# Kernel optimization log

Measured on AMD Instinct MI355X. Metric: run time of the kernel, lower is better.

The kernel has to match this reference:

```python
import jax, jax.numpy as jnp
import numpy as np

N = 50000      # nodes
D = 128        # in = hidden = out channels
L = 3          # num_layers
E = 320000     # edges per edge type
EPS_BN = 1e-5
EPS_NORM = 1e-12


def setup_inputs() -> dict:
    key = jax.random.key(0)
    ks = jax.random.split(key, 16)
    s = 1.0 / np.sqrt(D)
    inp = {}
    inp['x'] = jax.random.normal(ks[0], (N, D), jnp.float32)
    inp['edge_index0'] = jax.random.randint(ks[1], (2, E), 0, N, jnp.int32)
    inp['edge_index1'] = jax.random.randint(ks[2], (2, E), 0, N, jnp.int32)
    inp['W0'] = jax.random.normal(ks[3], (L, D, D), jnp.float32) * s
    inp['b0'] = jnp.zeros((L, D), jnp.float32)
    inp['W1'] = jax.random.normal(ks[4], (L, D, D), jnp.float32) * s
    inp['b1'] = jnp.zeros((L, D), jnp.float32)
    inp['gamma'] = jnp.ones((L, D), jnp.float32)
    inp['beta'] = jnp.zeros((L, D), jnp.float32)
    inp['emb1_W'] = jax.random.normal(ks[5], (D, D), jnp.float32) * s
    inp['emb1_b'] = jnp.zeros((D,), jnp.float32)
    inp['emb2_W'] = jax.random.normal(ks[6], (D, D), jnp.float32) * s
    inp['emb2_b'] = jnp.zeros((D,), jnp.float32)
    inp['ph1_Wa'] = jax.random.normal(ks[7], (D, D), jnp.float32) * s
    inp['ph1_ba'] = jnp.zeros((D,), jnp.float32)
    inp['ph1_Wb'] = jax.random.normal(ks[8], (D, D), jnp.float32) * s
    inp['ph1_bb'] = jnp.zeros((D,), jnp.float32)
    inp['ph2_Wa'] = jax.random.normal(ks[9], (D, D), jnp.float32) * s
    inp['ph2_ba'] = jnp.zeros((D,), jnp.float32)
    inp['ph2_Wb'] = jax.random.normal(ks[10], (D, D), jnp.float32) * s
    inp['ph2_bb'] = jnp.zeros((D,), jnp.float32)
    return inp


def _gcn(h_in, W, b, src, dst):
    # PyG GCNConv: add self-loops, symmetric deg^{-1/2} normalization, then scatter-add.
    h = h_in @ W                                   # [N, D]
    ones = jnp.ones(src.shape[0], h.dtype)
    deg = jax.ops.segment_sum(ones, dst, num_segments=N) + 1.0   # +1 self-loop
    dinv = jax.lax.rsqrt(deg)
    coef = (dinv[src] * dinv[dst])[:, None]        # [E, 1]
    agg = jax.ops.segment_sum(h[src] * coef, dst, num_segments=N)
    agg = agg + h * (dinv * dinv)[:, None]         # self-loop contribution
    return agg + b


def _bn(x, g, bt):
    # training-mode BatchNorm1d (batch statistics, biased variance)
    mu = jnp.mean(x, axis=0)
    var = jnp.mean(jnp.square(x - mu), axis=0)
    return (x - mu) * jax.lax.rsqrt(var + EPS_BN) * g + bt


def _l2norm(x):
    n = jnp.sqrt(jnp.sum(x * x, axis=1, keepdims=True))
    return x / jnp.maximum(n, EPS_NORM)


def reference(x, edge_index0, edge_index1, W0, b0, W1, b1, gamma, beta,
              emb1_W, emb1_b, emb2_W, emb2_b,
              ph1_Wa, ph1_ba, ph1_Wb, ph1_bb,
              ph2_Wa, ph2_ba, ph2_Wb, ph2_bb):
    s0, d0 = edge_index0[0], edge_index0[1]
    s1, d1 = edge_index1[0], edge_index1[1]
    h = x
    for i in range(L):
        # HeteroConv with aggr='sum': sum of the two edge-type GCNConv outputs
        h = _gcn(h, W0[i], b0[i], s0, d0) + _gcn(h, W1[i], b1[i], s1, d1)
        h = _bn(h, gamma[i], beta[i])
        if i < L - 1:
            h = jax.nn.relu(h)   # dropout omitted (deterministic / eval)
    e1 = jnp.tanh(h @ emb1_W + emb1_b)
    e2 = _l2norm(jnp.tanh(h @ emb2_W + emb2_b))
    p1 = _l2norm(jax.nn.relu(e1 @ ph1_Wa + ph1_ba) @ ph1_Wb + ph1_bb)
    p2 = _l2norm(jax.nn.relu(e2 @ ph2_Wa + ph2_ba) @ ph2_Wb + ph2_bb)
    return (e1, e2, p1, p2)
```

## Files before the change

### kernel.cpp

```cpp
#include <hip/hip_runtime.h>
#include <cstdint>
#include <cstddef>

#define D 128

typedef __attribute__((ext_vector_type(8))) short bf16x8;
typedef __attribute__((ext_vector_type(4))) float f32x4;
typedef __attribute__((ext_vector_type(8))) _Float16 f16x8;

__device__ __forceinline__ unsigned short f2bf(float f) {
  unsigned int u = __float_as_uint(f);
  unsigned int r = u + 0x7FFFu + ((u >> 16) & 1u);
  return (unsigned short)(r >> 16);
}
__device__ __forceinline__ float bf2f(unsigned short h) {
  return __uint_as_float((unsigned int)h << 16);
}
__device__ __forceinline__ float fast_tanh(float x) {
  float cx = fminf(fmaxf(x, -15.f), 15.f);
  float e = __expf(2.f * cx);
  return (e - 1.f) * __builtin_amdgcn_rcpf(e + 1.f);
}
union HU { _Float16 f; unsigned short u; };

struct WPtrs { const float* w[12]; };

__global__ __launch_bounds__(256) void packcount_kernel(
    WPtrs P, unsigned short* __restrict__ Wp,
    const int* __restrict__ d0, const int* __restrict__ d1,
    int* __restrict__ cnt, int E, int N, int packBlocks) {
  if ((int)blockIdx.x < packBlocks) {
    int tid = blockIdx.x * 256 + threadIdx.x;
    int m = tid >> 14;
    int r = tid & 16383;
    int b = r & 7, lane = (r >> 3) & 63, ks = (r >> 9) & 3, jt = r >> 11;
    int k = ks * 32 + ((lane >> 4) << 3) + b;
    int j = jt * 16 + (lane & 15);
    float w = P.w[m][k * 128 + j];
    if (m < 8) {
      unsigned short h = f2bf(w);
      Wp[m * 32768 + r] = h;
      Wp[m * 32768 + 16384 + r] = f2bf(w - bf2f(h));
    } else {
      HU hh, ll;
      hh.f = (_Float16)w;
      ll.f = (_Float16)(w - (float)hh.f);
      Wp[m * 32768 + r] = hh.u;
      Wp[m * 32768 + 16384 + r] = ll.u;
    }
  } else {
    int e = ((int)blockIdx.x - packBlocks) * 256 + threadIdx.x;
    if (e < E) {
      atomicAdd(&cnt[d0[e]], 1);
      atomicAdd(&cnt[N + d1[e]], 1);
    }
  }
}

__global__ __launch_bounds__(256) void scan_part_kernel(const int* __restrict__ cnt,
                                                        int* __restrict__ off,
                                                        int* __restrict__ bsum, int n2) {
  __shared__ int sh[256];
  int t = threadIdx.x;
  int i0 = blockIdx.x * 512 + 2 * t;
  int a0 = (i0 < n2) ? cnt[i0] : 0;
  int a1 = (i0 + 1 < n2) ? cnt[i0 + 1] : 0;
  int s = a0 + a1;
  sh[t] = s;
  __syncthreads();
  for (int d = 1; d < 256; d <<= 1) {
    int v = (t >= d) ? sh[t - d] : 0;
    __syncthreads();
    sh[t] += v;
    __syncthreads();
  }
  int p = sh[t] - s;
  if (i0 < n2) off[i0] = p;
  if (i0 + 1 < n2) off[i0 + 1] = p + a0;
  if (t == 255) bsum[blockIdx.x] = sh[255];
}

__global__ __launch_bounds__(256) void scan_bsum_kernel(int* __restrict__ bsum, int nb,
                                                        int* __restrict__ off_total) {
  __shared__ int sh[256];
  int t = threadIdx.x;
  int s = (t < nb) ? bsum[t] : 0;
  sh[t] = s;
  __syncthreads();
  for (int d = 1; d < 256; d <<= 1) {
    int v = (t >= d) ? sh[t - d] : 0;
    __syncthreads();
    sh[t] += v;
    __syncthreads();
  }
  if (t < nb) bsum[t] = sh[t] - s;
  if (t == 255) *off_total = sh[255];
}

__global__ __launch_bounds__(256) void scan_add_kernel(int* __restrict__ off,
                                                       const int* __restrict__ bsum,
                                                       int* __restrict__ cnt,
                                                       float* __restrict__ dinv, int n2) {
  int add = bsum[blockIdx.x];
  int base = blockIdx.x * 512;
#pragma unroll
  for (int u = 0; u < 2; u++) {
    int i = base + threadIdx.x + u * 256;
    if (i < n2) {
      off[i] += add;
      dinv[i] = rsqrtf((float)cnt[i] + 1.0f);
      cnt[i] = 0;
    }
  }
}

__device__ __forceinline__ void split8(const float vv[8], bf16x8& hh, bf16x8& hl) {
#pragma unroll
  for (int c = 0; c < 8; c++) {
    unsigned short h = f2bf(vv[c]);
    hh[c] = (short)h;
    hl[c] = (short)f2bf(vv[c] - bf2f(h));
  }
}

template <int BN>
__device__ __forceinline__ void mm_dual_body(
    int bid, const unsigned short* __restrict__ Wp, const float* __restrict__ Af,
    const float* __restrict__ stats, const float* __restrict__ g0,
    const float* __restrict__ bt0, const float* __restrict__ dinv,
    _Float16* __restrict__ tab0, _Float16* __restrict__ tab1,
    int n, int N, float invn) {
  __shared__ float bnsc[128], bnsh[128];
  if (BN) {
    int t = threadIdx.x;
    if (t < 128) {
      float s = 0.f, q = 0.f;
#pragma unroll
      for (int r = 0; r < 8; r++) { s += stats[r * 128 + t]; q += stats[1024 + r * 128 + t]; }
      float mu = s * invn, var = q * invn - mu * mu;
      float sc = g0[t] * rsqrtf(var + 1e-5f);
      bnsc[t] = sc; bnsh[t] = bt0[t] - mu * sc;
    }
    __syncthreads();
  }
  constexpr int WJT = 4, WIT = 4;
  const int lane = threadIdx.x & 63;
  const int wid = threadIdx.x >> 6;
  const int wj = wid % 4, wi = wid / 4;
  const int jtbase = wj * WJT;
  const int ibase = bid * 64 + wi * WIT * 16;
  const int lrow = lane & 15, lgrp = lane >> 4;

  int node[WIT];
  bool valid[WIT];
#pragma unroll
  for (int it = 0; it < WIT; it++) {
    int i = ibase + it * 16 + lrow;
    valid[it] = (i < n);
    node[it] = valid[it] ? i : (n - 1);
  }

  f32x4 acc[WJT][WIT];
#pragma unroll
  for (int jt = 0; jt < WJT; jt++)
#pragma unroll
    for (int it = 0; it < WIT; it++) acc[jt][it] = (f32x4){0.f, 0.f, 0.f, 0.f};

#pragma unroll
  for (int ks = 0; ks < 4; ks++) {
    float sck[8], shk[8];
    if (BN) {
      int cb = ks * 32 + lgrp * 8;
#pragma unroll
      for (int c = 0; c < 8; c++) { sck[c] = bnsc[cb + c]; shk[c] = bnsh[cb + c]; }
    }
    bf16x8 awh[WJT], awl[WJT];
#pragma unroll
    for (int jt = 0; jt < WJT; jt++) {
      int jg = jtbase + jt;
      const unsigned short* base = Wp + ((jg >= 8) ? 32768 : 0);
      size_t fo = (size_t)(((jg & 7) * 4 + ks) * 64 + lane) * 8;
      awh[jt] = *(const bf16x8*)(base + fo);
      awl[jt] = *(const bf16x8*)(base + fo + 16384);
    }
#pragma unroll
    for (int it = 0; it < WIT; it++) {
      const float* src = Af + (size_t)node[it] * 128 + ks * 32 + lgrp * 8;
      float4 u0 = *(const float4*)src;
      float4 u1 = *(const float4*)(src + 4);
      float vv[8] = {u0.x, u0.y, u0.z, u0.w, u1.x, u1.y, u1.z, u1.w};
      if (BN) {
#pragma unroll
        for (int c = 0; c < 8; c++) vv[c] = fmaxf(vv[c] * sck[c] + shk[c], 0.f);
      }
      bf16x8 bhh, bhl;
      split8(vv, bhh, bhl);
#pragma unroll
      for (int jt = 0; jt < WJT; jt++) {
        acc[jt][it] = __builtin_amdgcn_mfma_f32_16x16x32_bf16(awh[jt], bhh, acc[jt][it], 0, 0, 0);
        acc[jt][it] = __builtin_amdgcn_mfma_f32_16x16x32_bf16(awl[jt], bhh, acc[jt][it], 0, 0, 0);
        acc[jt][it] = __builtin_amdgcn_mfma_f32_16x16x32_bf16(awh[jt], bhl, acc[jt][it], 0, 0, 0);
      }
    }
  }

#pragma unroll
  for (int it = 0; it < WIT; it++) {
    if (!valid[it]) continue;
    float d0v = dinv[node[it]];
    float d1v = dinv[N + node[it]];
#pragma unroll
    for (int jt = 0; jt < WJT; jt++) {
      int jg = jtbase + jt;
      float s = (jg < 8) ? d0v : d1v;
      _Float16 o[4];
#pragma unroll
      for (int c = 0; c < 4; c++) o[c] = (_Float16)(acc[jt][it][c] * s);
      _Float16* base = (jg < 8)
          ? (tab0 + (size_t)node[it] * 128 + jg * 16)
          : (tab1 + (size_t)node[it] * 128 + (jg - 8) * 16);
      *(uint2*)(base + lgrp * 4) = *(uint2*)o;
    }
  }
}

__global__ __launch_bounds__(256) void mm_dual_k(
    const unsigned short* __restrict__ Wp, const float* __restrict__ Af,
    const float* __restrict__ stats, const float* __restrict__ g0,
    const float* __restrict__ bt0, const float* __restrict__ dinv,
    _Float16* __restrict__ tab0, _Float16* __restrict__ tab1,
    int n, int N, float invn) {
  mm_dual_body<1>(blockIdx.x, Wp, Af, stats, g0, bt0, dinv, tab0, tab1, n, N, invn);
}

__global__ __launch_bounds__(256) void fillmm0_kernel(
    const int* __restrict__ ei0, const int* __restrict__ ei1,
    const int* __restrict__ off, int* __restrict__ cnt, int* __restrict__ csr,
    int E, int fillBlocks,
    const unsigned short* __restrict__ Wp, const float* __restrict__ x,
    const float* __restrict__ dinv, _Float16* __restrict__ tab0,
    _Float16* __restrict__ tab1, int n, int N) {
  if ((int)blockIdx.x < fillBlocks) {
    int e = blockIdx.x * 256 + threadIdx.x;
    if (e < E) {
      int s = ei0[e], d = ei0[E + e];
      int p = atomicAdd(&cnt[d], 1);
      csr[off[d] + p] = s;
      s = ei1[e]; d = ei1[E + e];
      p = atomicAdd(&cnt[N + d], 1);
      csr[off[N + d] + p] = s;
    }
  } else {
    mm_dual_body<0>(blockIdx.x - fillBlocks, Wp, x, nullptr, nullptr, nullptr,
                    dinv, tab0, tab1, n, N, 0.f);
  }
}

__global__ __launch_bounds__(256) void gather_kernel(
    const _Float16* __restrict__ tab0, const _Float16* __restrict__ tab1,
    const float* __restrict__ dinv, const int* __restrict__ off,
    const int* __restrict__ csr,
    const float* __restrict__ b0, const float* __restrict__ b1,
    float* __restrict__ outh, float* __restrict__ stats, int n, int N) {
  __shared__ float reds[4][128];
  __shared__ float redq[4][128];
  int t = threadIdx.x;
  int g = t >> 4, l = t & 15;
  int node = blockIdx.x * 16 + g;
  bool valid = node < n;
  int nd = valid ? node : 0;
  const f16x8* t0 = (const f16x8*)tab0;
  const f16x8* t1 = (const f16x8*)tab1;
  float s0[8] = {0,0,0,0,0,0,0,0}, s1[8] = {0,0,0,0,0,0,0,0};
  if (valid) {
    f16x8 v = t0[(size_t)nd * 16 + l];
#pragma unroll
    for (int c = 0; c < 8; c++) s0[c] = (float)v[c];
    v = t1[(size_t)nd * 16 + l];
#pragma unroll
    for (int c = 0; c < 8; c++) s1[c] = (float)v[c];
  }
  int a = valid ? off[nd] : 0, b = valid ? off[nd + 1] : 0;
  int j = a;
  for (; j + 3 < b; j += 4) {
    int i0 = csr[j], i1 = csr[j + 1], i2 = csr[j + 2], i3 = csr[j + 3];
    f16x8 v0 = t0[(size_t)i0 * 16 + l];
    f16x8 v1 = t0[(size_t)i1 * 16 + l];
    f16x8 v2 = t0[(size_t)i2 * 16 + l];
    f16x8 v3 = t0[(size_t)i3 * 16 + l];
#pragma unroll
    for (int c = 0; c < 8; c++)
      s0[c] += ((float)v0[c] + (float)v1[c]) + ((float)v2[c] + (float)v3[c]);
  }
  for (; j < b; j++) {
    f16x8 va = t0[(size_t)csr[j] * 16 + l];
#pragma unroll
    for (int c = 0; c < 8; c++) s0[c] += (float)va[c];
  }
  a = valid ? off[N + nd] : 0; b = valid ? off[N + nd + 1] : 0;
  j = a;
  for (; j + 3 < b; j += 4) {
    int i0 = csr[j], i1 = csr[j + 1], i2 = csr[j + 2], i3 = csr[j + 3];
    f16x8 v0 = t1[(size_t)i0 * 16 + l];
    f16x8 v1 = t1[(size_t)i1 * 16 + l];
    f16x8 v2 = t1[(size_t)i2 * 16 + l];
    f16x8 v3 = t1[(size_t)i3 * 16 + l];
#pragma unroll
    for (int c = 0; c < 8; c++)
      s1[c] += ((float)v0[c] + (float)v1[c]) + ((float)v2[c] + (float)v3[c]);
  }
  for (; j < b; j++) {
    f16x8 va = t1[(size_t)csr[j] * 16 + l];
#pragma unroll
    for (int c = 0; c < 8; c++) s1[c] += (float)va[c];
  }
  float o[8] = {0,0,0,0,0,0,0,0};
  if (valid) {
    float d0 = dinv[nd], d1 = dinv[N + nd];
    const float4* B0 = (const float4*)(b0 + l * 8);
    const float4* B1 = (const float4*)(b1 + l * 8);
    float4 ba0 = B0[0], ba1 = B0[1], bb0 = B1[0], bb1 = B1[1];
    float bs[8] = {ba0.x + bb0.x, ba0.y + bb0.y, ba0.z + bb0.z, ba0.w + bb0.w,
                   ba1.x + bb1.x, ba1.y + bb1.y, ba1.z + bb1.z, ba1.w + bb1.w};
#pragma unroll
    for (int c = 0; c < 8; c++) o[c] = d0 * s0[c] + d1 * s1[c] + bs[c];
    float* dst = outh + (size_t)nd * 128 + l * 8;
    *(float4*)dst = make_float4(o[0], o[1], o[2], o[3]);
    *(float4*)(dst + 4) = make_float4(o[4], o[5], o[6], o[7]);
  }
  float sv[8], q[8];
#pragma unroll
  for (int c = 0; c < 8; c++) { sv[c] = o[c]; q[c] = o[c] * o[c]; }
#pragma unroll
  for (int c = 0; c < 8; c++) {
    sv[c] += __shfl_xor(sv[c], 16); sv[c] += __shfl_xor(sv[c], 32);
    q[c] += __shfl_xor(q[c], 16);  q[c] += __shfl_xor(q[c], 32);
  }
  int lane = t & 63, wid = t >> 6;
  if (lane < 16) {
#pragma unroll
    for (int c = 0; c < 8; c++) { reds[wid][lane * 8 + c] = sv[c]; redq[wid][lane * 8 + c] = q[c]; }
  }
  __syncthreads();
  if (t < 128) {
    float ts = reds[0][t] + reds[1][t] + reds[2][t] + reds[3][t];
    float tq = redq[0][t] + redq[1][t] + redq[2][t] + redq[3][t];
    int cp = blockIdx.x & 7;
    atomicAdd(&stats[cp * 128 + t], ts);
    atomicAdd(&stats[1024 + cp * 128 + t], tq);
  }
}

#define TPH 136
__global__ __launch_bounds__(256) void heads3_kernel(
    const unsigned short* __restrict__ Wp,
    const float* __restrict__ h, const float* __restrict__ stats,
    const float* __restrict__ g2, const float* __restrict__ bt2,
    const float* __restrict__ emb1_b, const float* __restrict__ emb2_b,
    const float* __restrict__ ph1_ba, const float* __restrict__ ph1_bb,
    const float* __restrict__ ph2_ba, const float* __restrict__ ph2_bb,
    float* __restrict__ out, int n, float invn) {
  __shared__ float bnsc[128], bnsh[128];
  __shared__ _Float16 tile[2][64 * TPH];
  __shared__ float l2red[2][4][16][2];
  const int t = threadIdx.x;
  if (t < 128) {
    float s = 0.f, q = 0.f;
#pragma unroll
    for (int r = 0; r < 8; r++) { s += stats[r * 128 + t]; q += stats[1024 + r * 128 + t]; }
    float mu = s * invn, var = q * invn - mu * mu;
    float sc = g2[t] * rsqrtf(var + 1e-5f);
    bnsc[t] = sc; bnsh[t] = bt2[t] - mu * sc;
  }
  __syncthreads();

  const int lane = t & 63, wid = t >> 6;
  const int wj = wid & 1, wh = wid >> 1;
  const int lrow = lane & 15, lgrp = lane >> 4;
  const int jtbase = wj * 4;
  const int base = blockIdx.x * 64;
  const size_t ND = (size_t)n * 128;
  _Float16* myt = &tile[wh][0];

  int node[4];
  bool valid[4];
#pragma unroll
  for (int it = 0; it < 4; it++) {
    int i = base + it * 16 + lrow;
    valid[it] = (i < n);
    node[it] = valid[it] ? i : (n - 1);
  }

  f32x4 acc[4][4];
  const unsigned short* slot;
  const float* bias;

  slot = Wp + (size_t)(6 + wh) * 32768;
  bias = wh ? emb2_b : emb1_b;
#pragma unroll
  for (int jt = 0; jt < 4; jt++) {
    float4 b4 = *(const float4*)(bias + (jtbase + jt) * 16 + lgrp * 4);
#pragma unroll
    for (int it = 0; it < 4; it++) acc[jt][it] = (f32x4){b4.x, b4.y, b4.z, b4.w};
  }
#pragma unroll
  for (int ks = 0; ks < 4; ks++) {
    int cb = ks * 32 + lgrp * 8;
    float sck[8], shk[8];
#pragma unroll
    for (int c = 0; c < 8; c++) { sck[c] = bnsc[cb + c]; shk[c] = bnsh[cb + c]; }
    bf16x8 awh[4], awl[4];
#pragma unroll
    for (int jt = 0; jt < 4; jt++) {
      size_t fo = (size_t)(((jtbase + jt) * 4 + ks) * 64 + lane) * 8;
      awh[jt] = *(const bf16x8*)(slot + fo);
      awl[jt] = *(const bf16x8*)(slot + fo + 16384);
    }
#pragma unroll
    for (int it = 0; it < 4; it++) {
      const float* src = h + (size_t)node[it] * 128 + cb;
      float4 u0 = *(const float4*)src;
      float4 u1 = *(const float4*)(src + 4);
      float vv[8] = {u0.x, u0.y, u0.z, u0.w, u1.x, u1.y, u1.z, u1.w};
#pragma unroll
      for (int c = 0; c < 8; c++) vv[c] = vv[c] * sck[c] + shk[c];
      bf16x8 bhh, bhl;
      split8(vv, bhh, bhl);
#pragma unroll
      for (int jt = 0; jt < 4; jt++) {
        acc[jt][it] = __builtin_amdgcn_mfma_f32_16x16x32_bf16(awh[jt], bhh, acc[jt][it], 0, 0, 0);
        acc[jt][it] = __builtin_amdgcn_mfma_f32_16x16x32_bf16(awl[jt], bhh, acc[jt][it], 0, 0, 0);
        acc[jt][it] = __builtin_amdgcn_mfma_f32_16x16x32_bf16(awh[jt], bhl, acc[jt][it], 0, 0, 0);
      }
    }
  }
#pragma unroll
  for (int jt = 0; jt < 4; jt++)
#pragma unroll
    for (int it = 0; it < 4; it++)
#pragma unroll
      for (int c = 0; c < 4; c++) acc[jt][it][c] = fast_tanh(acc[jt][it][c]);

  float rsv[4];
  if (wh == 1) {
#pragma unroll
    for (int it = 0; it < 4; it++) {
      float rs = 0.f;
#pragma unroll
      for (int jt = 0; jt < 4; jt++)
#pragma unroll
        for (int c = 0; c < 4; c++) rs += acc[jt][it][c] * acc[jt][it][c];
      rs += __shfl_xor(rs, 16);
      rs += __shfl_xor(rs, 32);
      rsv[it] = rs;
      if (lane < 16) l2red[1][it][lane][wj] = rs;
    }
  }
  __syncthreads();
  if (wh == 1) {
#pragma unroll
    for (int it = 0; it < 4; it++) {
      float full = rsv[it] + l2red[1][it][lrow][wj ^ 1];
      float scl = 1.f / fmaxf(sqrtf(full), 1e-12f);
#pragma unroll
      for (int jt = 0; jt < 4; jt++)
#pragma unroll
        for (int c = 0; c < 4; c++) acc[jt][it][c] *= scl;
    }
  }
#pragma unroll
  for (int it = 0; it < 4; it++) {
#pragma unroll
    for (int jt = 0; jt < 4; jt++) {
      if (valid[it])
        *(float4*)(out + (size_t)wh * ND + (size_t)node[it] * 128 + (jtbase + jt) * 16 + lgrp * 4) =
            make_float4(acc[jt][it][0], acc[jt][it][1], acc[jt][it][2], acc[jt][it][3]);
      _Float16 o4[4];
#pragma unroll
      for (int c = 0; c < 4; c++) o4[c] = (_Float16)acc[jt][it][c];
      *(uint2*)(myt + (it * 16 + lrow) * TPH + (jtbase + jt) * 16 + lgrp * 4) = *(uint2*)o4;
    }
  }
  __syncthreads();

  slot = Wp + (size_t)(8 + 2 * wh) * 32768;
  bias = wh ? ph2_ba : ph1_ba;
#pragma unroll
  for (int jt = 0; jt < 4; jt++) {
    float4 b4 = *(const float4*)(bias + (jtbase + jt) * 16 + lgrp * 4);
#pragma unroll
    for (int it = 0; it < 4; it++) acc[jt][it] = (f32x4){b4.x, b4.y, b4.z, b4.w};
  }
#pragma unroll
  for (int ks = 0; ks < 4; ks++) {
    f16x8 awh[4], awl[4];
#pragma unroll
    for (int jt = 0; jt < 4; jt++) {
      size_t fo = (size_t)(((jtbase + jt) * 4 + ks) * 64 + lane) * 8;
      awh[jt] = *(const f16x8*)(slot + fo);
      awl[jt] = *(const f16x8*)(slot + fo + 16384);
    }
#pragma unroll
    for (int it = 0; it < 4; it++) {
      f16x8 bh = *(const f16x8*)(myt + (it * 16 + lrow) * TPH + ks * 32 + lgrp * 8);
#pragma unroll
      for (int jt = 0; jt < 4; jt++) {
        acc[jt][it] = __builtin_amdgcn_mfma_f32_16x16x32_f16(awh[jt], bh, acc[jt][it], 0, 0, 0);
        acc[jt][it] = __builtin_amdgcn_mfma_f32_16x16x32_f16(awl[jt], bh, acc[jt][it], 0, 0, 0);
      }
    }
  }
#pragma unroll
  for (int jt = 0; jt < 4; jt++)
#pragma unroll
    for (int it = 0; it < 4; it++)
#pragma unroll
      for (int c = 0; c < 4; c++) acc[jt][it][c] = fmaxf(acc[jt][it][c], 0.f);
  __syncthreads();
#pragma unroll
  for (int it = 0; it < 4; it++)
#pragma unroll
    for (int jt = 0; jt < 4; jt++) {
      _Float16 o4[4];
#pragma unroll
      for (int c = 0; c < 4; c++) o4[c] = (_Float16)acc[jt][it][c];
      *(uint2*)(myt + (it * 16 + lrow) * TPH + (jtbase + jt) * 16 + lgrp * 4) = *(uint2*)o4;
    }
  __syncthreads();

  slot = Wp + (size_t)(9 + 2 * wh) * 32768;
  bias = wh ? ph2_bb : ph1_bb;
#pragma unroll
  for (int jt = 0; jt < 4; jt++) {
    float4 b4 = *(const float4*)(bias + (jtbase + jt) * 16 + lgrp * 4);
#pragma unroll
    for (int it = 0; it < 4; it++) acc[jt][it] = (f32x4){b4.x, b4.y, b4.z, b4.w};
  }
#pragma unroll
  for (int ks = 0; ks < 4; ks++) {
    f16x8 awh[4], awl[4];
#pragma unroll
    for (int jt = 0; jt < 4; jt++) {
      size_t fo = (size_t)(((jtbase + jt) * 4 + ks) * 64 + lane) * 8;
      awh[jt] = *(const f16x8*)(slot + fo);
      awl[jt] = *(const f16x8*)(slot + fo + 16384);
    }
#pragma unroll
    for (int it = 0; it < 4; it++) {
      f16x8 bh = *(const f16x8*)(myt + (it * 16 + lrow) * TPH + ks * 32 + lgrp * 8);
#pragma unroll
      for (int jt = 0; jt < 4; jt++) {
        acc[jt][it] = __builtin_amdgcn_mfma_f32_16x16x32_f16(awh[jt], bh, acc[jt][it], 0, 0, 0);
        acc[jt][it] = __builtin_amdgcn_mfma_f32_16x16x32_f16(awl[jt], bh, acc[jt][it], 0, 0, 0);
      }
    }
  }
#pragma unroll
  for (int it = 0; it < 4; it++) {
    float rs = 0.f;
#pragma unroll
    for (int jt = 0; jt < 4; jt++)
#pragma unroll
      for (int c = 0; c < 4; c++) rs += acc[jt][it][c] * acc[jt][it][c];
    rs += __shfl_xor(rs, 16);
    rs += __shfl_xor(rs, 32);
    rsv[it] = rs;
    if (lane < 16) l2red[wh][it][lane][wj] = rs;
  }
  __syncthreads();
#pragma unroll
  for (int it = 0; it < 4; it++) {
    float full = rsv[it] + l2red[wh][it][lrow][wj ^ 1];
    float scl = 1.f / fmaxf(sqrtf(full), 1e-12f);
    if (!valid[it]) continue;
#pragma unroll
    for (int jt = 0; jt < 4; jt++)
      *(float4*)(out + (size_t)(2 + wh) * ND + (size_t)node[it] * 128 + (jtbase + jt) * 16 + lgrp * 4) =
          make_float4(acc[jt][it][0] * scl, acc[jt][it][1] * scl,
                      acc[jt][it][2] * scl, acc[jt][it][3] * scl);
  }
}

extern "C" void kernel_launch(void* const* d_in, const int* in_sizes, int n_in,
                              void* d_out, int out_size, void* d_ws, size_t ws_size,
                              hipStream_t stream) {
  const float* x      = (const float*)d_in[0];
  const int*   ei0    = (const int*)d_in[1];
  const int*   ei1    = (const int*)d_in[2];
  const float* W0     = (const float*)d_in[3];
  const float* b0     = (const float*)d_in[4];
  const float* W1     = (const float*)d_in[5];
  const float* b1     = (const float*)d_in[6];
  const float* gamma  = (const float*)d_in[7];
  const float* beta   = (const float*)d_in[8];
  const float* emb1_W = (const float*)d_in[9];
  const float* emb1_b = (const float*)d_in[10];
  const float* emb2_W = (const float*)d_in[11];
  const float* emb2_b = (const float*)d_in[12];
  const float* ph1_Wa = (const float*)d_in[13];
  const float* ph1_ba = (const float*)d_in[14];
  const float* ph1_Wb = (const float*)d_in[15];
  const float* ph1_bb = (const float*)d_in[16];
  const float* ph2_Wa = (const float*)d_in[17];
  const float* ph2_ba = (const float*)d_in[18];
  const float* ph2_Wb = (const float*)d_in[19];
  const float* ph2_bb = (const float*)d_in[20];

  const int N = in_sizes[0] / D;
  const int E = in_sizes[1] / 2;
  const int N2 = 2 * N;
  const size_t ND = (size_t)N * D;
  const float invn = 1.0f / (float)N;
  float* out = (float*)d_out;

  char* p = (char*)d_ws;
  auto carve = [&](size_t bytes) -> void* {
    void* r = (void*)p;
    p += (bytes + 255) & ~(size_t)255;
    return r;
  };
  int*   cnt   = (int*)carve((size_t)N2 * 4);
  float* stats = (float*)carve((size_t)3 * 2048 * 4);
  size_t zbytes = (size_t)((char*)(stats + 3 * 2048) - (char*)cnt);
  int*   off   = (int*)carve((size_t)(N2 + 1) * 4);
  float* dinv  = (float*)carve((size_t)N2 * 4);
  int*   csr   = (int*)carve((size_t)2 * E * 4);
  int*   bsum  = (int*)carve(256 * 4);
  unsigned short* Wp = (unsigned short*)carve((size_t)12 * 32768 * 2);
  float* hbuf = (float*)carve(4 * ND);
  _Float16* tab0 = (_Float16*)carve(2 * ND);
  _Float16* tab1 = (_Float16*)carve(2 * ND);

  const int TPB = 256;
  const int packBlocks = 768;
  const int gridPC = packBlocks + (E + TPB - 1) / TPB;
  const int fillBlocks = (E + TPB - 1) / TPB;
  const int nbScan = (N2 + 511) / 512;
  const int gridDual = (N + 63) / 64;
  const int gridGath = (N + 15) / 16;
  const int gridH3 = (N + 63) / 64;

  WPtrs P;
  P.w[0] = W0;                     P.w[1] = W1;
  P.w[2] = W0 + (size_t)D * D;     P.w[3] = W1 + (size_t)D * D;
  P.w[4] = W0 + (size_t)2 * D * D; P.w[5] = W1 + (size_t)2 * D * D;
  P.w[6] = emb1_W; P.w[7] = emb2_W;
  P.w[8] = ph1_Wa; P.w[9] = ph1_Wb;
  P.w[10] = ph2_Wa; P.w[11] = ph2_Wb;

  hipMemsetAsync(cnt, 0, zbytes, stream);
  packcount_kernel<<<gridPC, TPB, 0, stream>>>(P, Wp, ei0 + E, ei1 + E, cnt, E, N, packBlocks);
  scan_part_kernel<<<nbScan, TPB, 0, stream>>>(cnt, off, bsum, N2);
  scan_bsum_kernel<<<1, TPB, 0, stream>>>(bsum, nbScan, off + N2);
  scan_add_kernel<<<nbScan, TPB, 0, stream>>>(off, bsum, cnt, dinv, N2);

  fillmm0_kernel<<<fillBlocks + gridDual, TPB, 0, stream>>>(
      ei0, ei1, off, cnt, csr, E, fillBlocks, Wp, x, dinv, tab0, tab1, N, N);
  gather_kernel<<<gridGath, TPB, 0, stream>>>(tab0, tab1, dinv, off, csr,
                                              b0, b1, hbuf, stats, N, N);
  for (int i = 1; i < 3; i++) {
    mm_dual_k<<<gridDual, TPB, 0, stream>>>(Wp + (size_t)(2 * i) * 32768, hbuf,
                                            stats + (size_t)(i - 1) * 2048,
                                            gamma + (i - 1) * D, beta + (i - 1) * D,
                                            dinv, tab0, tab1, N, N, invn);
    gather_kernel<<<gridGath, TPB, 0, stream>>>(tab0, tab1, dinv, off, csr,
                                                b0 + i * D, b1 + i * D, hbuf,
                                                stats + (size_t)i * 2048, N, N);
  }

  heads3_kernel<<<gridH3, TPB, 0, stream>>>(
      Wp, hbuf, stats + (size_t)2 * 2048, gamma + 2 * D, beta + 2 * D,
      emb1_b, emb2_b, ph1_ba, ph1_bb, ph2_ba, ph2_bb, out, N, invn);
}
```

Before: 329.1 us.

## Sort nodes by total degree so gather blocks process similar-degree nodes

Adds a degree histogram, a scan over its bins and an atomic bucket scatter that builds a node permutation ordered by combined in-degree. The gather kernel then handles nodes in that order, so the 16-node groups within a block have similar loop trip counts and less load imbalance. The cost is two extra kernel launches, atomics, an indirection read per node, and output writes plus neighbour-table reads that are less coalesced because consecutive groups now touch scattered node ids.

New measurement: 484.5 us. 47.2% more time.

```diff
diff --git a/kernel.cpp b/kernel.cpp
--- a/kernel.cpp
+++ b/kernel.cpp
@@ -114,6 +114,53 @@
   }
 }
 
+__global__ __launch_bounds__(256) void fillhist_kernel(
+    const int* __restrict__ ei0, const int* __restrict__ ei1,
+    const int* __restrict__ off, int* __restrict__ cnt,
+    int* __restrict__ csr, int* __restrict__ hist,
+    int E, int N, int fillBlocks, int histBlocks) {
+  if ((int)blockIdx.x < fillBlocks) {
+    int e = blockIdx.x * 256 + threadIdx.x;
+    if (e < E) {
+      int s = ei0[e], d = ei0[E + e];
+      int p = atomicAdd(&cnt[d], 1);
+      csr[off[d] + p] = s;
+      s = ei1[e]; d = ei1[E + e];
+      p = atomicAdd(&cnt[N + d], 1);
+      csr[off[N + d] + p] = s;
+    }
+  } else {
+    __shared__ int lh[512];
+    int t = threadIdx.x;
+    lh[t] = 0; lh[t + 256] = 0;
+    __syncthreads();
+    int stride = histBlocks * 256;
+    for (int i = ((int)blockIdx.x - fillBlocks) * 256 + t; i < N; i += stride) {
+      int key = (off[i + 1] - off[i]) + (off[N + i + 1] - off[N + i]);
+      atomicAdd(&lh[key < 511 ? key : 511], 1);
+    }
+    __syncthreads();
+    if (lh[t]) atomicAdd(&hist[t], lh[t]);
+    if (lh[t + 256]) atomicAdd(&hist[t + 256], lh[t + 256]);
+  }
+}
+
+__global__ __launch_bounds__(512) void binscan_kernel(const int* __restrict__ hist,
+                                                      int* __restrict__ cursor) {
+  __shared__ int sh[512];
+  int t = threadIdx.x;
+  int s = hist[t];
+  sh[t] = s;
+  __syncthreads();
+  for (int d = 1; d < 512; d <<= 1) {
+    int v = (t >= d) ? sh[t - d] : 0;
+    __syncthreads();
+    sh[t] += v;
+    __syncthreads();
+  }
+  cursor[t] = sh[t] - s;
+}
+
 __device__ __forceinline__ void split8(const float vv[8], bf16x8& hh, bf16x8& hl) {
 #pragma unroll
   for (int c = 0; c < 8; c++) {
@@ -233,25 +280,22 @@
   mm_dual_body<1>(blockIdx.x, Wp, Af, stats, g0, bt0, dinv, tab0, tab1, n, N, invn);
 }
 
-__global__ __launch_bounds__(256) void fillmm0_kernel(
-    const int* __restrict__ ei0, const int* __restrict__ ei1,
-    const int* __restrict__ off, int* __restrict__ cnt, int* __restrict__ csr,
-    int E, int fillBlocks,
+__global__ __launch_bounds__(256) void scatmm0_kernel(
+    const int* __restrict__ off, int* __restrict__ cursor, int* __restrict__ order,
+    int sortBlocks,
     const unsigned short* __restrict__ Wp, const float* __restrict__ x,
     const float* __restrict__ dinv, _Float16* __restrict__ tab0,
     _Float16* __restrict__ tab1, int n, int N) {
-  if ((int)blockIdx.x < fillBlocks) {
-    int e = blockIdx.x * 256 + threadIdx.x;
-    if (e < E) {
-      int s = ei0[e], d = ei0[E + e];
-      int p = atomicAdd(&cnt[d], 1);
-      csr[off[d] + p] = s;
-      s = ei1[e]; d = ei1[E + e];
-      p = atomicAdd(&cnt[N + d], 1);
-      csr[off[N + d] + p] = s;
+  if ((int)blockIdx.x < sortBlocks) {
+    int stride = sortBlocks * 256;
+    for (int i = (int)blockIdx.x * 256 + threadIdx.x; i < N; i += stride) {
+      int key = (off[i + 1] - off[i]) + (off[N + i + 1] - off[N + i]);
+      int b = key < 511 ? key : 511;
+      int pos = atomicAdd(&cursor[b], 1);
+      order[pos] = i;
     }
   } else {
-    mm_dual_body<0>(blockIdx.x - fillBlocks, Wp, x, nullptr, nullptr, nullptr,
+    mm_dual_body<0>(blockIdx.x - sortBlocks, Wp, x, nullptr, nullptr, nullptr,
                     dinv, tab0, tab1, n, N, 0.f);
   }
 }
@@ -259,16 +303,16 @@
 __global__ __launch_bounds__(256) void gather_kernel(
     const _Float16* __restrict__ tab0, const _Float16* __restrict__ tab1,
     const float* __restrict__ dinv, const int* __restrict__ off,
-    const int* __restrict__ csr,
+    const int* __restrict__ csr, const int* __restrict__ order,
     const float* __restrict__ b0, const float* __restrict__ b1,
     float* __restrict__ outh, float* __restrict__ stats, int n, int N) {
   __shared__ float reds[4][128];
   __shared__ float redq[4][128];
   int t = threadIdx.x;
   int g = t >> 4, l = t & 15;
-  int node = blockIdx.x * 16 + g;
-  bool valid = node < n;
-  int nd = valid ? node : 0;
+  int pos = blockIdx.x * 16 + g;
+  bool valid = pos < n;
+  int nd = valid ? order[pos] : 0;
   const f16x8* t0 = (const f16x8*)tab0;
   const f16x8* t1 = (const f16x8*)tab1;
   float s0[8] = {0,0,0,0,0,0,0,0}, s1[8] = {0,0,0,0,0,0,0,0};
@@ -621,7 +665,10 @@
   };
   int*   cnt   = (int*)carve((size_t)N2 * 4);
   float* stats = (float*)carve((size_t)3 * 2048 * 4);
-  size_t zbytes = (size_t)((char*)(stats + 3 * 2048) - (char*)cnt);
+  int*   hist  = (int*)carve(512 * 4);
+  size_t zbytes = (size_t)((char*)(hist + 512) - (char*)cnt);
+  int*   cursor = (int*)carve(512 * 4);
+  int*   order  = (int*)carve((size_t)N * 4);
   int*   off   = (int*)carve((size_t)(N2 + 1) * 4);
   float* dinv  = (float*)carve((size_t)N2 * 4);
   int*   csr   = (int*)carve((size_t)2 * E * 4);
@@ -635,6 +682,8 @@
   const int packBlocks = 768;
   const int gridPC = packBlocks + (E + TPB - 1) / TPB;
   const int fillBlocks = (E + TPB - 1) / TPB;
+  const int histBlocks = 32;
+  const int sortBlocks = 32;
   const int nbScan = (N2 + 511) / 512;
   const int gridDual = (N + 63) / 64;
   const int gridGath = (N + 15) / 16;
@@ -653,21 +702,22 @@
   scan_part_kernel<<<nbScan, TPB, 0, stream>>>(cnt, off, bsum, N2);
   scan_bsum_kernel<<<1, TPB, 0, stream>>>(bsum, nbScan, off + N2);
   scan_add_kernel<<<nbScan, TPB, 0, stream>>>(off, bsum, cnt, dinv, N2);
-
-  fillmm0_kernel<<<fillBlocks + gridDual, TPB, 0, stream>>>(
-      ei0, ei1, off, cnt, csr, E, fillBlocks, Wp, x, dinv, tab0, tab1, N, N);
-  gather_kernel<<<gridGath, TPB, 0, stream>>>(tab0, tab1, dinv, off, csr,
+  fillhist_kernel<<<fillBlocks + histBlocks, TPB, 0, stream>>>(
+      ei0, ei1, off, cnt, csr, hist, E, N, fillBlocks, histBlocks);
+  binscan_kernel<<<1, 512, 0, stream>>>(hist, cursor);
+  scatmm0_kernel<<<sortBlocks + gridDual, TPB, 0, stream>>>(
+      off, cursor, order, sortBlocks, Wp, x, dinv, tab0, tab1, N, N);
+  gather_kernel<<<gridGath, TPB, 0, stream>>>(tab0, tab1, dinv, off, csr, order,
                                               b0, b1, hbuf, stats, N, N);
   for (int i = 1; i < 3; i++) {
     mm_dual_k<<<gridDual, TPB, 0, stream>>>(Wp + (size_t)(2 * i) * 32768, hbuf,
                                             stats + (size_t)(i - 1) * 2048,
                                             gamma + (i - 1) * D, beta + (i - 1) * D,
                                             dinv, tab0, tab1, N, N, invn);
-    gather_kernel<<<gridGath, TPB, 0, stream>>>(tab0, tab1, dinv, off, csr,
+    gather_kernel<<<gridGath, TPB, 0, stream>>>(tab0, tab1, dinv, off, csr, order,
                                                 b0 + i * D, b1 + i * D, hbuf,
                                                 stats + (size_t)i * 2048, N, N);
   }
-
   heads3_kernel<<<gridH3, TPB, 0, stream>>>(
       Wp, hbuf, stats + (size_t)2 * 2048, gamma + 2 * D, beta + 2 * D,
       emb1_b, emb2_b, ph1_ba, ph1_bb, ph2_ba, ph2_bb, out, N, invn);
```

## Split fused fill/matmul kernel and interleave both edge-type gathers in one loop

Applied to the files above, without the earlier changes.

The combined CSR-fill plus first-layer matmul launch is split back into a separate fill kernel and a templated mm_dual kernel launched on its own. The gather kernel now walks both edge types' neighbor lists in one predicated loop, issuing four loads from each table per iteration to raise memory-level parallelism. Splitting the launches adds one kernel launch and removes overlap between the fill and matmul blocks. The interleaved loop wastes loads on padded lanes when one list is shorter than the other.

New measurement: 348.5 us. +5.9%, slower.

```diff
diff --git a/kernel.cpp b/kernel.cpp
--- a/kernel.cpp
+++ b/kernel.cpp
@@ -114,6 +114,20 @@
   }
 }
 
+__global__ void fill_kernel(const int* __restrict__ ei0, const int* __restrict__ ei1,
+                            const int* __restrict__ off, int* __restrict__ cnt,
+                            int* __restrict__ csr, int E, int N) {
+  int e = blockIdx.x * blockDim.x + threadIdx.x;
+  if (e < E) {
+    int s = ei0[e], d = ei0[E + e];
+    int p = atomicAdd(&cnt[d], 1);
+    csr[off[d] + p] = s;
+    s = ei1[e]; d = ei1[E + e];
+    p = atomicAdd(&cnt[N + d], 1);
+    csr[off[N + d] + p] = s;
+  }
+}
+
 __device__ __forceinline__ void split8(const float vv[8], bf16x8& hh, bf16x8& hl) {
 #pragma unroll
   for (int c = 0; c < 8; c++) {
@@ -124,8 +138,8 @@
 }
 
 template <int BN>
-__device__ __forceinline__ void mm_dual_body(
-    int bid, const unsigned short* __restrict__ Wp, const float* __restrict__ Af,
+__global__ __launch_bounds__(256) void mm_dual(
+    const unsigned short* __restrict__ Wp, const float* __restrict__ Af,
     const float* __restrict__ stats, const float* __restrict__ g0,
     const float* __restrict__ bt0, const float* __restrict__ dinv,
     _Float16* __restrict__ tab0, _Float16* __restrict__ tab1,
@@ -148,7 +162,7 @@
   const int wid = threadIdx.x >> 6;
   const int wj = wid % 4, wi = wid / 4;
   const int jtbase = wj * WJT;
-  const int ibase = bid * 64 + wi * WIT * 16;
+  const int ibase = blockIdx.x * 64 + wi * WIT * 16;
   const int lrow = lane & 15, lgrp = lane >> 4;
 
   int node[WIT];
@@ -221,38 +235,6 @@
           : (tab1 + (size_t)node[it] * 128 + (jg - 8) * 16);
       *(uint2*)(base + lgrp * 4) = *(uint2*)o;
     }
-  }
-}
-
-__global__ __launch_bounds__(256) void mm_dual_k(
-    const unsigned short* __restrict__ Wp, const float* __restrict__ Af,
-    const float* __restrict__ stats, const float* __restrict__ g0,
-    const float* __restrict__ bt0, const float* __restrict__ dinv,
-    _Float16* __restrict__ tab0, _Float16* __restrict__ tab1,
-    int n, int N, float invn) {
-  mm_dual_body<1>(blockIdx.x, Wp, Af, stats, g0, bt0, dinv, tab0, tab1, n, N, invn);
-}
-
-__global__ __launch_bounds__(256) void fillmm0_kernel(
-    const int* __restrict__ ei0, const int* __restrict__ ei1,
-    const int* __restrict__ off, int* __restrict__ cnt, int* __restrict__ csr,
-    int E, int fillBlocks,
-    const unsigned short* __restrict__ Wp, const float* __restrict__ x,
-    const float* __restrict__ dinv, _Float16* __restrict__ tab0,
-    _Float16* __restrict__ tab1, int n, int N) {
-  if ((int)blockIdx.x < fillBlocks) {
-    int e = blockIdx.x * 256 + threadIdx.x;
-    if (e < E) {
-      int s = ei0[e], d = ei0[E + e];
-      int p = atomicAdd(&cnt[d], 1);
-      csr[off[d] + p] = s;
-      s = ei1[e]; d = ei1[E + e];
-      p = atomicAdd(&cnt[N + d], 1);
-      csr[off[N + d] + p] = s;
-    }
-  } else {
-    mm_dual_body<0>(blockIdx.x - fillBlocks, Wp, x, nullptr, nullptr, nullptr,
-                    dinv, tab0, tab1, n, N, 0.f);
   }
 }
 
@@ -280,39 +262,38 @@
 #pragma unroll
     for (int c = 0; c < 8; c++) s1[c] = (float)v[c];
   }
-  int a = valid ? off[nd] : 0, b = valid ? off[nd + 1] : 0;
-  int j = a;
-  for (; j + 3 < b; j += 4) {
-    int i0 = csr[j], i1 = csr[j + 1], i2 = csr[j + 2], i3 = csr[j + 3];
-    f16x8 v0 = t0[(size_t)i0 * 16 + l];
-    f16x8 v1 = t0[(size_t)i1 * 16 + l];
-    f16x8 v2 = t0[(size_t)i2 * 16 + l];
-    f16x8 v3 = t0[(size_t)i3 * 16 + l];
-#pragma unroll
-    for (int c = 0; c < 8; c++)
-      s0[c] += ((float)v0[c] + (float)v1[c]) + ((float)v2[c] + (float)v3[c]);
-  }
-  for (; j < b; j++) {
-    f16x8 va = t0[(size_t)csr[j] * 16 + l];
-#pragma unroll
-    for (int c = 0; c < 8; c++) s0[c] += (float)va[c];
-  }
-  a = valid ? off[N + nd] : 0; b = valid ? off[N + nd + 1] : 0;
-  j = a;
-  for (; j + 3 < b; j += 4) {
-    int i0 = csr[j], i1 = csr[j + 1], i2 = csr[j + 2], i3 = csr[j + 3];
-    f16x8 v0 = t1[(size_t)i0 * 16 + l];
-    f16x8 v1 = t1[(size_t)i1 * 16 + l];
-    f16x8 v2 = t1[(size_t)i2 * 16 + l];
-    f16x8 v3 = t1[(size_t)i3 * 16 + l];
-#pragma unroll
-    for (int c = 0; c < 8; c++)
-      s1[c] += ((float)v0[c] + (float)v1[c]) + ((float)v2[c] + (float)v3[c]);
-  }
-  for (; j < b; j++) {
-    f16x8 va = t1[(size_t)csr[j] * 16 + l];
-#pragma unroll
-    for (int c = 0; c < 8; c++) s1[c] += (float)va[c];
+  int j0 = valid ? off[nd] : 0, e0 = valid ? off[nd + 1] : 0;
+  int j1 = valid ? off[N + nd] : 0, e1 = valid ? off[N + nd + 1] : 0;
+  while (j0 < e0 || j1 < e1) {
+    int idx0[4], idx1[4];
+    bool p0[4], p1[4];
+#pragma unroll
+    for (int k = 0; k < 4; k++) {
+      int jj = j0 + k;
+      p0[k] = jj < e0;
+      idx0[k] = nd;
+      if (p0[k]) idx0[k] = csr[jj];
+      jj = j1 + k;
+      p1[k] = jj < e1;
+      idx1[k] = nd;
+      if (p1[k]) idx1[k] = csr[jj];
+    }
+    f16x8 v0[4], v1[4];
+#pragma unroll
+    for (int k = 0; k < 4; k++) {
+      v0[k] = t0[(size_t)idx0[k] * 16 + l];
+      v1[k] = t1[(size_t)idx1[k] * 16 + l];
+    }
+#pragma unroll
+    for (int k = 0; k < 4; k++) {
+#pragma unroll
+      for (int c = 0; c < 8; c++) {
+        s0[c] += p0[k] ? (float)v0[k][c] : 0.f;
+        s1[c] += p1[k] ? (float)v1[k][c] : 0.f;
+      }
+    }
+    j0 = (j0 + 4 < e0) ? j0 + 4 : e0;
+    j1 = (j1 + 4 < e1) ? j1 + 4 : e1;
   }
   float o[8] = {0,0,0,0,0,0,0,0};
   if (valid) {
@@ -634,7 +615,7 @@
   const int TPB = 256;
   const int packBlocks = 768;
   const int gridPC = packBlocks + (E + TPB - 1) / TPB;
-  const int fillBlocks = (E + TPB - 1) / TPB;
+  const int gridE = (E + TPB - 1) / TPB;
   const int nbScan = (N2 + 511) / 512;
   const int gridDual = (N + 63) / 64;
   const int gridGath = (N + 15) / 16;
@@ -653,21 +634,21 @@
   scan_part_kernel<<<nbScan, TPB, 0, stream>>>(cnt, off, bsum, N2);
   scan_bsum_kernel<<<1, TPB, 0, stream>>>(bsum, nbScan, off + N2);
   scan_add_kernel<<<nbScan, TPB, 0, stream>>>(off, bsum, cnt, dinv, N2);
-
-  fillmm0_kernel<<<fillBlocks + gridDual, TPB, 0, stream>>>(
-      ei0, ei1, off, cnt, csr, E, fillBlocks, Wp, x, dinv, tab0, tab1, N, N);
+  fill_kernel<<<gridE, TPB, 0, stream>>>(ei0, ei1, off, cnt, csr, E, N);
+
+  mm_dual<0><<<gridDual, TPB, 0, stream>>>(Wp, x, nullptr, nullptr, nullptr,
+                                           dinv, tab0, tab1, N, N, invn);
   gather_kernel<<<gridGath, TPB, 0, stream>>>(tab0, tab1, dinv, off, csr,
                                               b0, b1, hbuf, stats, N, N);
   for (int i = 1; i < 3; i++) {
-    mm_dual_k<<<gridDual, TPB, 0, stream>>>(Wp + (size_t)(2 * i) * 32768, hbuf,
-                                            stats + (size_t)(i - 1) * 2048,
-                                            gamma + (i - 1) * D, beta + (i - 1) * D,
-                                            dinv, tab0, tab1, N, N, invn);
+    mm_dual<1><<<gridDual, TPB, 0, stream>>>(Wp + (size_t)(2 * i) * 32768, hbuf,
+                                             stats + (size_t)(i - 1) * 2048,
+                                             gamma + (i - 1) * D, beta + (i - 1) * D,
+                                             dinv, tab0, tab1, N, N, invn);
     gather_kernel<<<gridGath, TPB, 0, stream>>>(tab0, tab1, dinv, off, csr,
                                                 b0 + i * D, b1 + i * D, hbuf,
                                                 stats + (size_t)i * 2048, N, N);
   }
-
   heads3_kernel<<<gridH3, TPB, 0, stream>>>(
       Wp, hbuf, stats + (size_t)2 * 2048, gamma + 2 * D, beta + 2 * D,
       emb1_b, emb2_b, ph1_ba, ph1_bb, ph2_ba, ph2_bb, out, N, invn);
```

## Record atomic ranks in count pass, merge scan kernels, use packed bf16 convert

Applied to the files above, without the earlier changes.

The counting pass now stores the slot returned by each atomicAdd as a per-edge rank, so the CSR fill no longer repeats atomics and instead writes directly at off[d]+rank. The block-sum scan and the add pass are merged into one kernel that every block recomputes redundantly, which removes one launch and the cnt reset. The bf16 hi/lo split is rewritten with the packed v_cvt_pk_bf16_f32 instruction in place of manual rounding. The cost is two extra E-sized int arrays that are written and then read back.

Result: faster. 310.9 us (-5.5%).

```diff
diff --git a/kernel.cpp b/kernel.cpp
--- a/kernel.cpp
+++ b/kernel.cpp
@@ -7,6 +7,7 @@
 typedef __attribute__((ext_vector_type(8))) short bf16x8;
 typedef __attribute__((ext_vector_type(4))) float f32x4;
 typedef __attribute__((ext_vector_type(8))) _Float16 f16x8;
+typedef __attribute__((ext_vector_type(4))) unsigned int u32x4;
 
 __device__ __forceinline__ unsigned short f2bf(float f) {
   unsigned int u = __float_as_uint(f);
@@ -23,12 +24,30 @@
 }
 union HU { _Float16 f; unsigned short u; };
 
+__device__ __forceinline__ void split8(const float vv[8], bf16x8& hh, bf16x8& hl) {
+  u32x4 ph, pl;
+#pragma unroll
+  for (int i = 0; i < 4; i++) {
+    unsigned int p;
+    asm("v_cvt_pk_bf16_f32 %0, %1, %2" : "=v"(p) : "v"(vv[2 * i]), "v"(vv[2 * i + 1]));
+    ph[i] = p;
+    float r0 = vv[2 * i] - __uint_as_float(p << 16);
+    float r1 = vv[2 * i + 1] - __uint_as_float(p & 0xFFFF0000u);
+    unsigned int q;
+    asm("v_cvt_pk_bf16_f32 %0, %1, %2" : "=v"(q) : "v"(r0), "v"(r1));
+    pl[i] = q;
+  }
+  hh = __builtin_bit_cast(bf16x8, ph);
+  hl = __builtin_bit_cast(bf16x8, pl);
+}
+
 struct WPtrs { const float* w[12]; };
 
 __global__ __launch_bounds__(256) void packcount_kernel(
     WPtrs P, unsigned short* __restrict__ Wp,
     const int* __restrict__ d0, const int* __restrict__ d1,
-    int* __restrict__ cnt, int E, int N, int packBlocks) {
+    int* __restrict__ cnt, int* __restrict__ rank0, int* __restrict__ rank1,
+    int E, int N, int packBlocks) {
   if ((int)blockIdx.x < packBlocks) {
     int tid = blockIdx.x * 256 + threadIdx.x;
     int m = tid >> 14;
@@ -51,8 +70,8 @@
   } else {
     int e = ((int)blockIdx.x - packBlocks) * 256 + threadIdx.x;
     if (e < E) {
-      atomicAdd(&cnt[d0[e]], 1);
-      atomicAdd(&cnt[N + d1[e]], 1);
+      rank0[e] = atomicAdd(&cnt[d0[e]], 1);
+      rank1[e] = atomicAdd(&cnt[N + d1[e]], 1);
     }
   }
 }
@@ -80,8 +99,11 @@
   if (t == 255) bsum[blockIdx.x] = sh[255];
 }
 
-__global__ __launch_bounds__(256) void scan_bsum_kernel(int* __restrict__ bsum, int nb,
-                                                        int* __restrict__ off_total) {
+__global__ __launch_bounds__(256) void scan_addm_kernel(int* __restrict__ off,
+                                                        const int* __restrict__ bsum,
+                                                        const int* __restrict__ cnt,
+                                                        float* __restrict__ dinv,
+                                                        int n2, int nb) {
   __shared__ int sh[256];
   int t = threadIdx.x;
   int s = (t < nb) ? bsum[t] : 0;
@@ -93,33 +115,16 @@
     sh[t] += v;
     __syncthreads();
   }
-  if (t < nb) bsum[t] = sh[t] - s;
-  if (t == 255) *off_total = sh[255];
-}
-
-__global__ __launch_bounds__(256) void scan_add_kernel(int* __restrict__ off,
-                                                       const int* __restrict__ bsum,
-                                                       int* __restrict__ cnt,
-                                                       float* __restrict__ dinv, int n2) {
-  int add = bsum[blockIdx.x];
+  if (blockIdx.x == 0 && t == 0) off[n2] = sh[nb - 1];
+  int add = (blockIdx.x > 0) ? sh[blockIdx.x - 1] : 0;
   int base = blockIdx.x * 512;
 #pragma unroll
   for (int u = 0; u < 2; u++) {
-    int i = base + threadIdx.x + u * 256;
+    int i = base + t + u * 256;
     if (i < n2) {
       off[i] += add;
       dinv[i] = rsqrtf((float)cnt[i] + 1.0f);
-      cnt[i] = 0;
-    }
-  }
-}
-
-__device__ __forceinline__ void split8(const float vv[8], bf16x8& hh, bf16x8& hl) {
-#pragma unroll
-  for (int c = 0; c < 8; c++) {
-    unsigned short h = f2bf(vv[c]);
-    hh[c] = (short)h;
-    hl[c] = (short)f2bf(vv[c] - bf2f(h));
+    }
   }
 }
 
@@ -235,7 +240,8 @@
 
 __global__ __launch_bounds__(256) void fillmm0_kernel(
     const int* __restrict__ ei0, const int* __restrict__ ei1,
-    const int* __restrict__ off, int* __restrict__ cnt, int* __restrict__ csr,
+    const int* __restrict__ off, const int* __restrict__ rank0,
+    const int* __restrict__ rank1, int* __restrict__ csr,
     int E, int fillBlocks,
     const unsigned short* __restrict__ Wp, const float* __restrict__ x,
     const float* __restrict__ dinv, _Float16* __restrict__ tab0,
@@ -244,11 +250,9 @@
     int e = blockIdx.x * 256 + threadIdx.x;
     if (e < E) {
       int s = ei0[e], d = ei0[E + e];
-      int p = atomicAdd(&cnt[d], 1);
-      csr[off[d] + p] = s;
+      csr[off[d] + rank0[e]] = s;
       s = ei1[e]; d = ei1[E + e];
-      p = atomicAdd(&cnt[N + d], 1);
-      csr[off[N + d] + p] = s;
+      csr[off[N + d] + rank1[e]] = s;
     }
   } else {
     mm_dual_body<0>(blockIdx.x - fillBlocks, Wp, x, nullptr, nullptr, nullptr,
@@ -625,6 +629,8 @@
   int*   off   = (int*)carve((size_t)(N2 + 1) * 4);
   float* dinv  = (float*)carve((size_t)N2 * 4);
   int*   csr   = (int*)carve((size_t)2 * E * 4);
+  int*   rank0 = (int*)carve((size_t)E * 4);
+  int*   rank1 = (int*)carve((size_t)E * 4);
   int*   bsum  = (int*)carve(256 * 4);
   unsigned short* Wp = (unsigned short*)carve((size_t)12 * 32768 * 2);
   float* hbuf = (float*)carve(4 * ND);
@@ -649,13 +655,13 @@
   P.w[10] = ph2_Wa; P.w[11] = ph2_Wb;
 
   hipMemsetAsync(cnt, 0, zbytes, stream);
-  packcount_kernel<<<gridPC, TPB, 0, stream>>>(P, Wp, ei0 + E, ei1 + E, cnt, E, N, packBlocks);
+  packcount_kernel<<<gridPC, TPB, 0, stream>>>(P, Wp, ei0 + E, ei1 + E, cnt,
+                                               rank0, rank1, E, N, packBlocks);
   scan_part_kernel<<<nbScan, TPB, 0, stream>>>(cnt, off, bsum, N2);
-  scan_bsum_kernel<<<1, TPB, 0, stream>>>(bsum, nbScan, off + N2);
-  scan_add_kernel<<<nbScan, TPB, 0, stream>>>(off, bsum, cnt, dinv, N2);
+  scan_addm_kernel<<<nbScan, TPB, 0, stream>>>(off, bsum, cnt, dinv, N2, nbScan);
 
   fillmm0_kernel<<<fillBlocks + gridDual, TPB, 0, stream>>>(
-      ei0, ei1, off, cnt, csr, E, fillBlocks, Wp, x, dinv, tab0, tab1, N, N);
+      ei0, ei1, off, rank0, rank1, csr, E, fillBlocks, Wp, x, dinv, tab0, tab1, N, N);
   gather_kernel<<<gridGath, TPB, 0, stream>>>(tab0, tab1, dinv, off, csr,
                                               b0, b1, hbuf, stats, N, N);
   for (int i = 1; i < 3; i++) {
@@ -667,7 +673,6 @@
                                                 b0 + i * D, b1 + i * D, hbuf,
                                                 stats + (size_t)i * 2048, N, N);
   }
-
   heads3_kernel<<<gridH3, TPB, 0, stream>>>(
       Wp, hbuf, stats + (size_t)2 * 2048, gamma + 2 * D, beta + 2 * D,
       emb1_b, emb2_b, ph1_ba, ph1_bb, ph2_ba, ph2_bb, out, N, invn);
```
